# Optimization experiments

Measured on AMD Instinct MI355X. Metric: run time of the kernel, lower is better.

The kernel has to match this reference:

```python
import jax, jax.numpy as jnp
import numpy as np

P, B, N, M, D_LAT = 4, 32, 2048, 512, 128
BETA = 1e-3
BIG = 1e9  # sentinel for masked-out pairwise distances


def quat_to_rotmat(q):
    # q: (..., 4) quaternion (w, x, y, z), normalized then converted
    q = q / jnp.linalg.norm(q, axis=-1, keepdims=True)
    w, x, y, z = q[..., 0], q[..., 1], q[..., 2], q[..., 3]
    R = jnp.stack([
        1 - 2 * (y * y + z * z), 2 * (x * y - w * z), 2 * (x * z + w * y),
        2 * (x * y + w * z), 1 - 2 * (x * x + z * z), 2 * (y * z - w * x),
        2 * (x * z - w * y), 2 * (y * z + w * x), 1 - 2 * (x * x + y * y),
    ], axis=-1)
    return R.reshape(q.shape[:-1] + (3, 3))


def setup_inputs() -> dict:
    key = jax.random.key(0)
    ks = jax.random.split(key, 8)
    return {
        'ipt': jax.random.normal(ks[0], (B, N, 3), jnp.float32),
        'opt': jax.random.normal(ks[1], (P, B, M, 3), jnp.float32),
        'trans': jax.random.normal(ks[2], (P, B, 3), jnp.float32),
        'rots': jax.random.normal(ks[3], (P, B, 4), jnp.float32),
        'probs': jax.random.uniform(ks[4], (P, B, 1), jnp.float32),
        'idx': jax.random.randint(ks[5], (B, N), 0, P),
        'mu': jax.random.normal(ks[6], (B, D_LAT), jnp.float32),
        'logvar': jax.random.normal(ks[7], (B, D_LAT), jnp.float32),
    }


def _parts_distance(ipt, opt, trans, rots, probs, idx):
    # Masked, fully-batched equivalent of the original python double loop:
    # index_select by (idx==i) + _remove_zero_rows are expressed as boolean
    # masks; empty part/sample combinations are excluded via `valid`.
    chamfer_d = 0.0
    coverage = 0.0
    quality = 0.0
    num = 0.0
    nonzero_x = jnp.any(ipt != 0, axis=-1)  # (B, N)
    for i in range(P):  # fixed small part count, structurally distinct slices
        y = opt[i]                                   # (B, M, 3)
        mask_y = jnp.any(y != 0, axis=-1)            # (B, M) _remove_zero_rows
        mx = (idx == i) & nonzero_x                  # (B, N) part selection
        # transform_to_primitives_centric_system: x_local = R (x - t)
        R = quat_to_rotmat(rots[i])                  # (B, 3, 3)
        x = jnp.einsum('bij,bnj->bni', R, ipt - trans[i][:, None, :])
        # pairwise squared distances, (B, N, M)
        D = jnp.sum((x[:, :, None, :] - y[:, None, :, :]) ** 2, axis=-1)
        nx = jnp.sum(mx, axis=-1)                    # (B,)
        ny = jnp.sum(mask_y, axis=-1)                # (B,)
        # quality: mean over valid x of min distance to valid y
        qual = jnp.sum(jnp.where(mx, jnp.min(jnp.where(mask_y[:, None, :], D, BIG), axis=-1), 0.0), axis=-1) / jnp.maximum(nx, 1)
        # coverage: mean over valid y of min distance to valid x
        cov = jnp.sum(jnp.where(mask_y, jnp.min(jnp.where(mx[:, :, None], D, BIG), axis=-2), 0.0), axis=-1) / jnp.maximum(ny, 1)
        cd = qual + cov                              # symmetric chamfer
        valid = (nx > 0) & (ny > 0)                  # x.size(0)!=0 and y.size(0)!=0
        w = jnp.where(valid, probs[i][:, 0], 0.0)    # prob-weighted sum over batch
        n = jnp.sum(valid).astype(jnp.float32)
        has = (n > 0).astype(jnp.float32)
        inv_n = has / jnp.maximum(n, 1.0)
        chamfer_d = chamfer_d + jnp.sum(w * cd) * inv_n
        coverage = coverage + jnp.sum(w * cov) * inv_n
        quality = quality + jnp.sum(w * qual) * inv_n
        num = num + has
    inv_num = 1.0 / jnp.maximum(num, 1.0)
    return chamfer_d * inv_num, coverage * inv_num, quality * inv_num


def KL(mu, logvar):
    # standard VAE KL: sum over latent, mean over batch
    return -0.5 * jnp.sum(1.0 + logvar - mu ** 2 - jnp.exp(logvar)) / mu.shape[0]


def reference(ipt, opt, trans, rots, probs, idx, mu, logvar):
    cds, covs, quals = _parts_distance(ipt, opt, trans, rots, probs, idx)
    kld = KL(mu, logvar)
    return (cds + BETA * kld, cds, covs, quals, kld)
```

## Files before the change

kernel.cpp:

```cpp
#include <hip/hip_runtime.h>
#include <math.h>

#define PP 4
#define BB 32
#define PB (PP * BB)
#define NN 2048
#define MM 512
#define DLAT 128
#define BETA_C 1e-3f
#define BIGV 1e9f
#define SENT 1e8f
#define THREADS 512
#define NWAVE (THREADS / 64)
#define NCHUNK 2
#define QCH (NN / NCHUNK)
#define CCH (MM / NCHUNK)
#define XMAX (NN + 32)

__device__ float g_ws[8 * PB];

__device__ __forceinline__ int wave_compact_slot(bool sel, int* s_cnt, int tid) {
    unsigned long long bal = __ballot(sel);
    int lofs = __popcll(bal & ((1ull << (tid & 63)) - 1ull));
    int base = 0;
    if ((tid & 63) == 0 && bal) base = atomicAdd(s_cnt, __popcll(bal));
    base = __shfl(base, 0);
    return base + lofs;
}

__global__ __launch_bounds__(THREADS) void parts_kernel(
    const float* __restrict__ ipt,
    const float* __restrict__ opt,
    const float* __restrict__ trans,
    const float* __restrict__ rots,
    const int*   __restrict__ idx)
{
    const int b = blockIdx.x;
    const int i = blockIdx.y;
    const int z = blockIdx.z;
    const int tid = threadIdx.x;
    const int lane = tid & 63;
    const int w = tid >> 6;

    __shared__ float Rm[12];
    __shared__ int s_nx, s_ny;
    __shared__ __align__(16) float syx[MM], syy[MM], syz[MM];
    __shared__ __align__(16) float sxx[XMAX], sxy[XMAX], sxz[XMAX];
    __shared__ float pmin[NWAVE][256];
    __shared__ float red[NWAVE];

    if (tid == 0) {
        s_nx = 0;
        s_ny = 0;
        const float* q = rots + (i * BB + b) * 4;
        float qw = q[0], qx = q[1], qy = q[2], qz = q[3];
        float inv = 1.0f / sqrtf(qw * qw + qx * qx + qy * qy + qz * qz);
        qw *= inv; qx *= inv; qy *= inv; qz *= inv;
        Rm[0] = 1.0f - 2.0f * (qy * qy + qz * qz);
        Rm[1] = 2.0f * (qx * qy - qw * qz);
        Rm[2] = 2.0f * (qx * qz + qw * qy);
        Rm[3] = 2.0f * (qx * qy + qw * qz);
        Rm[4] = 1.0f - 2.0f * (qx * qx + qz * qz);
        Rm[5] = 2.0f * (qy * qz - qw * qx);
        Rm[6] = 2.0f * (qx * qz - qw * qy);
        Rm[7] = 2.0f * (qy * qz + qw * qx);
        Rm[8] = 1.0f - 2.0f * (qx * qx + qy * qy);
        const float* t = trans + (i * BB + b) * 3;
        Rm[9] = t[0]; Rm[10] = t[1]; Rm[11] = t[2];
    }
    __syncthreads();

    const float R0 = Rm[0], R1 = Rm[1], R2 = Rm[2];
    const float R3 = Rm[3], R4 = Rm[4], R5 = Rm[5];
    const float R6 = Rm[6], R7 = Rm[7], R8 = Rm[8];
    const float t0 = Rm[9], t1 = Rm[10], t2 = Rm[11];
    const size_t optbase = ((size_t)i * BB + b) * MM;
    const int pb = i * BB + b;

    float sum = 0.0f;

    if (z < NCHUNK) {
        for (int m = tid; m < MM; m += THREADS) {
            const float* y = opt + (optbase + m) * 3;
            float yx = y[0], yy = y[1], yz = y[2];
            bool v = (yx != 0.0f) | (yy != 0.0f) | (yz != 0.0f);
            if (!v) { yx = SENT; yy = SENT; yz = SENT; }
            syx[m] = yx; syy[m] = yy; syz[m] = yz;
        }
        const int n0 = z * QCH;
        for (int n = n0 + tid; n < n0 + QCH; n += THREADS) {
            const float* p = ipt + ((size_t)b * NN + n) * 3;
            float px = p[0], py = p[1], pz = p[2];
            bool nz = (px != 0.0f) | (py != 0.0f) | (pz != 0.0f);
            bool sel = nz && (idx[b * NN + n] == i);
            int pos = wave_compact_slot(sel, &s_nx, tid);
            if (sel) {
                px -= t0; py -= t1; pz -= t2;
                sxx[pos] = R0 * px + R1 * py + R2 * pz;
                sxy[pos] = R3 * px + R4 * py + R5 * pz;
                sxz[pos] = R6 * px + R7 * py + R8 * pz;
            }
        }
        __syncthreads();
        const int nxc = s_nx;
        const int y0 = w * (MM / NWAVE);

        for (int base = 0; base < nxc; base += 256) {
            float px[4], py[4], pz[4], mn[4];
#pragma unroll
            for (int s = 0; s < 4; ++s) {
                int k = base + s * 64 + lane;
                bool a = (k < nxc);
                px[s] = a ? sxx[k] : SENT;
                py[s] = a ? sxy[k] : SENT;
                pz[s] = a ? sxz[k] : SENT;
                mn[s] = BIGV;
            }
#pragma unroll 4
            for (int j = 0; j < MM / NWAVE; j += 4) {
                float4 yx = *reinterpret_cast<const float4*>(syx + y0 + j);
                float4 yy = *reinterpret_cast<const float4*>(syy + y0 + j);
                float4 yz = *reinterpret_cast<const float4*>(syz + y0 + j);
#pragma unroll
                for (int s = 0; s < 4; ++s) {
                    float dx0 = px[s] - yx.x, dy0 = py[s] - yy.x, dz0 = pz[s] - yz.x;
                    float dx1 = px[s] - yx.y, dy1 = py[s] - yy.y, dz1 = pz[s] - yz.y;
                    float dx2 = px[s] - yx.z, dy2 = py[s] - yy.z, dz2 = pz[s] - yz.z;
                    float dx3 = px[s] - yx.w, dy3 = py[s] - yy.w, dz3 = pz[s] - yz.w;
                    float d0 = dx0 * dx0 + dy0 * dy0 + dz0 * dz0;
                    float d1 = dx1 * dx1 + dy1 * dy1 + dz1 * dz1;
                    float d2 = dx2 * dx2 + dy2 * dy2 + dz2 * dz2;
                    float d3 = dx3 * dx3 + dy3 * dy3 + dz3 * dz3;
                    mn[s] = fminf(mn[s], fminf(fminf(d0, d1), fminf(d2, d3)));
                }
            }
#pragma unroll
            for (int s = 0; s < 4; ++s) pmin[w][s * 64 + lane] = mn[s];
            __syncthreads();
            if (tid < 256) {
                int j = tid;
                if (base + j < nxc) {
                    float m = pmin[0][j];
#pragma unroll
                    for (int ww = 1; ww < NWAVE; ++ww) m = fminf(m, pmin[ww][j]);
                    sum += m;
                }
            }
            __syncthreads();
        }

        for (int off = 32; off > 0; off >>= 1) sum += __shfl_down(sum, off);
        if (lane == 0) red[w] = sum;
        __syncthreads();
        if (tid == 0) {
            float tot = 0.0f;
            for (int ww = 0; ww < NWAVE; ++ww) tot += red[ww];
            g_ws[(0 + z) * PB + pb] = tot;
            g_ws[(4 + z) * PB + pb] = (float)s_nx;
        }
    } else {
        const int c = z - NCHUNK;
        if (tid < CCH) {
            const float* y = opt + (optbase + c * CCH + tid) * 3;
            float yx = y[0], yy = y[1], yz = y[2];
            bool v = (yx != 0.0f) | (yy != 0.0f) | (yz != 0.0f);
            if (!v) { yx = SENT; yy = SENT; yz = SENT; }
            syx[tid] = yx; syy[tid] = yy; syz[tid] = yz;
            unsigned long long bal = __ballot(v);
            if (lane == 0) atomicAdd(&s_ny, __popcll(bal));
        }
        for (int n = tid; n < NN; n += THREADS) {
            const float* p = ipt + ((size_t)b * NN + n) * 3;
            float px = p[0], py = p[1], pz = p[2];
            bool nz = (px != 0.0f) | (py != 0.0f) | (pz != 0.0f);
            bool sel = nz && (idx[b * NN + n] == i);
            int pos = wave_compact_slot(sel, &s_nx, tid);
            if (sel) {
                px -= t0; py -= t1; pz -= t2;
                sxx[pos] = R0 * px + R1 * py + R2 * pz;
                sxy[pos] = R3 * px + R4 * py + R5 * pz;
                sxz[pos] = R6 * px + R7 * py + R8 * pz;
            }
        }
        __syncthreads();
        const int nx = s_nx;
        const int ny = s_ny;
        const int nx32 = (nx + 31) & ~31;
        if (tid < nx32 - nx) {
            sxx[nx + tid] = SENT; sxy[nx + tid] = SENT; sxz[nx + tid] = SENT;
        }
        __syncthreads();

        float qx[4], qy[4], qz[4], mn[4];
#pragma unroll
        for (int s = 0; s < 4; ++s) {
            int j = s * 64 + lane;
            qx[s] = syx[j]; qy[s] = syy[j]; qz[s] = syz[j];
            mn[s] = BIGV;
        }
        const int q = nx32 / NWAVE;
        const int x0 = w * q;
#pragma unroll 4
        for (int k = 0; k < q; k += 4) {
            float4 xx = *reinterpret_cast<const float4*>(sxx + x0 + k);
            float4 xy = *reinterpret_cast<const float4*>(sxy + x0 + k);
            float4 xz = *reinterpret_cast<const float4*>(sxz + x0 + k);
#pragma unroll
            for (int s = 0; s < 4; ++s) {
                float dx0 = qx[s] - xx.x, dy0 = qy[s] - xy.x, dz0 = qz[s] - xz.x;
                float dx1 = qx[s] - xx.y, dy1 = qy[s] - xy.y, dz1 = qz[s] - xz.y;
                float dx2 = qx[s] - xx.z, dy2 = qy[s] - xy.z, dz2 = qz[s] - xz.z;
                float dx3 = qx[s] - xx.w, dy3 = qy[s] - xy.w, dz3 = qz[s] - xz.w;
                float d0 = dx0 * dx0 + dy0 * dy0 + dz0 * dz0;
                float d1 = dx1 * dx1 + dy1 * dy1 + dz1 * dz1;
                float d2 = dx2 * dx2 + dy2 * dy2 + dz2 * dz2;
                float d3 = dx3 * dx3 + dy3 * dy3 + dz3 * dz3;
                mn[s] = fminf(mn[s], fminf(fminf(d0, d1), fminf(d2, d3)));
            }
        }
#pragma unroll
        for (int s = 0; s < 4; ++s) pmin[w][s * 64 + lane] = mn[s];
        __syncthreads();
        if (tid < CCH) {
            int j = tid;
            if (syx[j] != SENT) {
                float m = pmin[0][j];
#pragma unroll
                for (int ww = 1; ww < NWAVE; ++ww) m = fminf(m, pmin[ww][j]);
                sum += m;
            }
        }
        __syncthreads();

        for (int off = 32; off > 0; off >>= 1) sum += __shfl_down(sum, off);
        if (lane == 0) red[w] = sum;
        __syncthreads();
        if (tid == 0) {
            float tot = 0.0f;
            for (int ww = 0; ww < NWAVE; ++ww) tot += red[ww];
            g_ws[(2 + c) * PB + pb] = tot;
            g_ws[(6 + c) * PB + pb] = (float)ny;
        }
    }
}

__global__ __launch_bounds__(256) void finalize_kernel(
    const float* __restrict__ probs,
    const float* __restrict__ mu,
    const float* __restrict__ logvar,
    float* __restrict__ out)
{
    const int tid = threadIdx.x;
    __shared__ float red[4];
    __shared__ float s_wq[PB], s_wc[PB], s_val[PB];

    const float4* mu4 = reinterpret_cast<const float4*>(mu);
    const float4* lv4 = reinterpret_cast<const float4*>(logvar);
    float kls = 0.0f;
    for (int t = tid; t < BB * DLAT / 4; t += 256) {
        float4 m4 = mu4[t], l4 = lv4[t];
        kls += (1.0f + l4.x - m4.x * m4.x - expf(l4.x))
             + (1.0f + l4.y - m4.y * m4.y - expf(l4.y))
             + (1.0f + l4.z - m4.z * m4.z - expf(l4.z))
             + (1.0f + l4.w - m4.w * m4.w - expf(l4.w));
    }
    for (int off = 32; off > 0; off >>= 1) kls += __shfl_down(kls, off);
    if ((tid & 63) == 0) red[tid >> 6] = kls;

    if (tid < PB) {
        float qs  = g_ws[0 * PB + tid] + g_ws[1 * PB + tid];
        float cs  = g_ws[2 * PB + tid] + g_ws[3 * PB + tid];
        float nxf = g_ws[4 * PB + tid] + g_ws[5 * PB + tid];
        float nyf = g_ws[6 * PB + tid] + g_ws[7 * PB + tid];
        bool valid = (nxf > 0.0f) && (nyf > 0.0f);
        float w = valid ? probs[tid] : 0.0f;
        s_wq[tid] = w * (qs / fmaxf(nxf, 1.0f));
        s_wc[tid] = w * (cs / fmaxf(nyf, 1.0f));
        s_val[tid] = valid ? 1.0f : 0.0f;
    }
    __syncthreads();

    if (tid == 0) {
        float kld = -0.5f * (red[0] + red[1] + red[2] + red[3]) / (float)BB;
        float ch = 0.0f, cov = 0.0f, qu = 0.0f, num = 0.0f;
        for (int i = 0; i < PP; ++i) {
            float sq = 0.0f, sc = 0.0f, n = 0.0f;
            for (int bb = 0; bb < BB; ++bb) {
                sq += s_wq[i * BB + bb];
                sc += s_wc[i * BB + bb];
                n += s_val[i * BB + bb];
            }
            float has = (n > 0.0f) ? 1.0f : 0.0f;
            float invn = has / fmaxf(n, 1.0f);
            qu += sq * invn;
            cov += sc * invn;
            ch += (sq + sc) * invn;
            num += has;
        }
        float invnum = 1.0f / fmaxf(num, 1.0f);
        float cds = ch * invnum;
        out[0] = cds + BETA_C * kld;
        out[1] = cds;
        out[2] = cov * invnum;
        out[3] = qu * invnum;
        out[4] = kld;
    }
}

extern "C" void kernel_launch(void* const* d_in, const int* in_sizes, int n_in,
                              void* d_out, int out_size, void* d_ws, size_t ws_size,
                              hipStream_t stream) {
    const float* ipt    = (const float*)d_in[0];
    const float* opt    = (const float*)d_in[1];
    const float* trans  = (const float*)d_in[2];
    const float* rots   = (const float*)d_in[3];
    const float* probs  = (const float*)d_in[4];
    const int*   idx    = (const int*)d_in[5];
    const float* mu     = (const float*)d_in[6];
    const float* logvar = (const float*)d_in[7];
    float* out = (float*)d_out;
    (void)d_ws; (void)ws_size; (void)in_sizes; (void)n_in; (void)out_size;

    dim3 grid(BB, PP, 2 * NCHUNK);
    parts_kernel<<<grid, THREADS, 0, stream>>>(ipt, opt, trans, rots, idx);
    finalize_kernel<<<1, 256, 0, stream>>>(probs, mu, logvar, out);
}
```

Baseline: 95.23 us.

## Fuse finalize into parts kernel via last-block atomic and split work finer

Merges the finalize kernel into the main kernel: each block bumps a global counter after a threadfence, and the last block to finish does the KL and weighted reduction. This removes a second launch and its gap. The grid also goes from 4 to 8 chunks per (part, batch), with 256-thread blocks and 2 points per lane instead of 4, to raise block count and occupancy. The cost is more redundant per-block loading and compaction of the input points, plus the atomic-counter handshake.

```diff
diff --git a/kernel.cpp b/kernel.cpp
--- a/kernel.cpp
+++ b/kernel.cpp
@@ -10,30 +10,37 @@
 #define BETA_C 1e-3f
 #define BIGV 1e9f
 #define SENT 1e8f
-#define THREADS 512
-#define NWAVE (THREADS / 64)
-#define NCHUNK 2
-#define QCH (NN / NCHUNK)
-#define CCH (MM / NCHUNK)
-#define XMAX (NN + 32)
-
-__device__ float g_ws[8 * PB];
-
-__device__ __forceinline__ int wave_compact_slot(bool sel, int* s_cnt, int tid) {
+#define THREADS 256
+#define NWAVE 4
+#define QCHUNKS 4
+#define CCHUNKS 4
+#define QCH (NN / QCHUNKS)
+#define CCH (MM / CCHUNKS)
+#define TOTALBLK (BB * PP * (QCHUNKS + CCHUNKS))
+#define XMAX (NN + 16)
+
+__device__ float g_ws[16 * PB];
+__device__ int g_done;
+
+__device__ __forceinline__ int wave_compact_slot(bool sel, int* s_cnt, int lane) {
     unsigned long long bal = __ballot(sel);
-    int lofs = __popcll(bal & ((1ull << (tid & 63)) - 1ull));
+    int lofs = __popcll(bal & ((1ull << lane) - 1ull));
     int base = 0;
-    if ((tid & 63) == 0 && bal) base = atomicAdd(s_cnt, __popcll(bal));
+    if (lane == 0 && bal) base = atomicAdd(s_cnt, __popcll(bal));
     base = __shfl(base, 0);
     return base + lofs;
 }
 
-__global__ __launch_bounds__(THREADS) void parts_kernel(
+__global__ __launch_bounds__(THREADS) void fused_kernel(
     const float* __restrict__ ipt,
     const float* __restrict__ opt,
     const float* __restrict__ trans,
     const float* __restrict__ rots,
-    const int*   __restrict__ idx)
+    const int*   __restrict__ idx,
+    const float* __restrict__ probs,
+    const float* __restrict__ mu,
+    const float* __restrict__ logvar,
+    float* __restrict__ out)
 {
     const int b = blockIdx.x;
     const int i = blockIdx.y;
@@ -43,10 +50,10 @@
     const int w = tid >> 6;
 
     __shared__ float Rm[12];
-    __shared__ int s_nx, s_ny;
+    __shared__ int s_nx, s_ny, s_last;
     __shared__ __align__(16) float syx[MM], syy[MM], syz[MM];
     __shared__ __align__(16) float sxx[XMAX], sxy[XMAX], sxz[XMAX];
-    __shared__ float pmin[NWAVE][256];
+    __shared__ float pmin[NWAVE][128];
     __shared__ float red[NWAVE];
 
     if (tid == 0) {
@@ -79,7 +86,7 @@
 
     float sum = 0.0f;
 
-    if (z < NCHUNK) {
+    if (z < QCHUNKS) {
         for (int m = tid; m < MM; m += THREADS) {
             const float* y = opt + (optbase + m) * 3;
             float yx = y[0], yy = y[1], yz = y[2];
@@ -93,7 +100,7 @@
             float px = p[0], py = p[1], pz = p[2];
             bool nz = (px != 0.0f) | (py != 0.0f) | (pz != 0.0f);
             bool sel = nz && (idx[b * NN + n] == i);
-            int pos = wave_compact_slot(sel, &s_nx, tid);
+            int pos = wave_compact_slot(sel, &s_nx, lane);
             if (sel) {
                 px -= t0; py -= t1; pz -= t2;
                 sxx[pos] = R0 * px + R1 * py + R2 * pz;
@@ -105,24 +112,24 @@
         const int nxc = s_nx;
         const int y0 = w * (MM / NWAVE);
 
-        for (int base = 0; base < nxc; base += 256) {
-            float px[4], py[4], pz[4], mn[4];
-#pragma unroll
-            for (int s = 0; s < 4; ++s) {
+        for (int base = 0; base < nxc; base += 128) {
+            float px[2], py[2], pz[2], mn[2];
+            bool act[2];
+#pragma unroll
+            for (int s = 0; s < 2; ++s) {
                 int k = base + s * 64 + lane;
-                bool a = (k < nxc);
-                px[s] = a ? sxx[k] : SENT;
-                py[s] = a ? sxy[k] : SENT;
-                pz[s] = a ? sxz[k] : SENT;
+                act[s] = (k < nxc);
+                px[s] = act[s] ? sxx[k] : SENT;
+                py[s] = act[s] ? sxy[k] : SENT;
+                pz[s] = act[s] ? sxz[k] : SENT;
                 mn[s] = BIGV;
             }
-#pragma unroll 4
             for (int j = 0; j < MM / NWAVE; j += 4) {
                 float4 yx = *reinterpret_cast<const float4*>(syx + y0 + j);
                 float4 yy = *reinterpret_cast<const float4*>(syy + y0 + j);
                 float4 yz = *reinterpret_cast<const float4*>(syz + y0 + j);
 #pragma unroll
-                for (int s = 0; s < 4; ++s) {
+                for (int s = 0; s < 2; ++s) {
                     float dx0 = px[s] - yx.x, dy0 = py[s] - yy.x, dz0 = pz[s] - yz.x;
                     float dx1 = px[s] - yx.y, dy1 = py[s] - yy.y, dz1 = pz[s] - yz.y;
                     float dx2 = px[s] - yx.z, dy2 = py[s] - yy.z, dz2 = pz[s] - yz.z;
@@ -135,16 +142,13 @@
                 }
             }
 #pragma unroll
-            for (int s = 0; s < 4; ++s) pmin[w][s * 64 + lane] = mn[s];
+            for (int s = 0; s < 2; ++s) pmin[w][s * 64 + lane] = mn[s];
             __syncthreads();
-            if (tid < 256) {
-                int j = tid;
-                if (base + j < nxc) {
-                    float m = pmin[0][j];
-#pragma unroll
-                    for (int ww = 1; ww < NWAVE; ++ww) m = fminf(m, pmin[ww][j]);
-                    sum += m;
-                }
+            if (tid < 128 && base + tid < nxc) {
+                float m = pmin[0][tid];
+#pragma unroll
+                for (int ww = 1; ww < NWAVE; ++ww) m = fminf(m, pmin[ww][tid]);
+                sum += m;
             }
             __syncthreads();
         }
@@ -153,13 +157,12 @@
         if (lane == 0) red[w] = sum;
         __syncthreads();
         if (tid == 0) {
-            float tot = 0.0f;
-            for (int ww = 0; ww < NWAVE; ++ww) tot += red[ww];
+            float tot = red[0] + red[1] + red[2] + red[3];
             g_ws[(0 + z) * PB + pb] = tot;
-            g_ws[(4 + z) * PB + pb] = (float)s_nx;
+            g_ws[(8 + z) * PB + pb] = (float)s_nx;
         }
     } else {
-        const int c = z - NCHUNK;
+        const int c = z - QCHUNKS;
         if (tid < CCH) {
             const float* y = opt + (optbase + c * CCH + tid) * 3;
             float yx = y[0], yy = y[1], yz = y[2];
@@ -174,7 +177,7 @@
             float px = p[0], py = p[1], pz = p[2];
             bool nz = (px != 0.0f) | (py != 0.0f) | (pz != 0.0f);
             bool sel = nz && (idx[b * NN + n] == i);
-            int pos = wave_compact_slot(sel, &s_nx, tid);
+            int pos = wave_compact_slot(sel, &s_nx, lane);
             if (sel) {
                 px -= t0; py -= t1; pz -= t2;
                 sxx[pos] = R0 * px + R1 * py + R2 * pz;
@@ -185,28 +188,27 @@
         __syncthreads();
         const int nx = s_nx;
         const int ny = s_ny;
-        const int nx32 = (nx + 31) & ~31;
-        if (tid < nx32 - nx) {
+        const int nx16 = (nx + 15) & ~15;
+        if (tid < nx16 - nx) {
             sxx[nx + tid] = SENT; sxy[nx + tid] = SENT; sxz[nx + tid] = SENT;
         }
         __syncthreads();
 
-        float qx[4], qy[4], qz[4], mn[4];
-#pragma unroll
-        for (int s = 0; s < 4; ++s) {
+        float qx[2], qy[2], qz[2], mn[2];
+#pragma unroll
+        for (int s = 0; s < 2; ++s) {
             int j = s * 64 + lane;
             qx[s] = syx[j]; qy[s] = syy[j]; qz[s] = syz[j];
             mn[s] = BIGV;
         }
-        const int q = nx32 / NWAVE;
+        const int q = nx16 / NWAVE;
         const int x0 = w * q;
-#pragma unroll 4
         for (int k = 0; k < q; k += 4) {
             float4 xx = *reinterpret_cast<const float4*>(sxx + x0 + k);
             float4 xy = *reinterpret_cast<const float4*>(sxy + x0 + k);
             float4 xz = *reinterpret_cast<const float4*>(sxz + x0 + k);
 #pragma unroll
-            for (int s = 0; s < 4; ++s) {
+            for (int s = 0; s < 2; ++s) {
                 float dx0 = qx[s] - xx.x, dy0 = qy[s] - xy.x, dz0 = qz[s] - xz.x;
                 float dx1 = qx[s] - xx.y, dy1 = qy[s] - xy.y, dz1 = qz[s] - xz.y;
                 float dx2 = qx[s] - xx.z, dy2 = qy[s] - xy.z, dz2 = qz[s] - xz.z;
@@ -219,16 +221,13 @@
             }
         }
 #pragma unroll
-        for (int s = 0; s < 4; ++s) pmin[w][s * 64 + lane] = mn[s];
-        __syncthreads();
-        if (tid < CCH) {
-            int j = tid;
-            if (syx[j] != SENT) {
-                float m = pmin[0][j];
-#pragma unroll
-                for (int ww = 1; ww < NWAVE; ++ww) m = fminf(m, pmin[ww][j]);
-                sum += m;
-            }
+        for (int s = 0; s < 2; ++s) pmin[w][s * 64 + lane] = mn[s];
+        __syncthreads();
+        if (tid < CCH && syx[tid] != SENT) {
+            float m = pmin[0][tid];
+#pragma unroll
+            for (int ww = 1; ww < NWAVE; ++ww) m = fminf(m, pmin[ww][tid]);
+            sum += m;
         }
         __syncthreads();
 
@@ -236,28 +235,26 @@
         if (lane == 0) red[w] = sum;
         __syncthreads();
         if (tid == 0) {
-            float tot = 0.0f;
-            for (int ww = 0; ww < NWAVE; ++ww) tot += red[ww];
-            g_ws[(2 + c) * PB + pb] = tot;
-            g_ws[(6 + c) * PB + pb] = (float)ny;
-        }
-    }
-}
-
-__global__ __launch_bounds__(256) void finalize_kernel(
-    const float* __restrict__ probs,
-    const float* __restrict__ mu,
-    const float* __restrict__ logvar,
-    float* __restrict__ out)
-{
-    const int tid = threadIdx.x;
-    __shared__ float red[4];
-    __shared__ float s_wq[PB], s_wc[PB], s_val[PB];
+            float tot = red[0] + red[1] + red[2] + red[3];
+            g_ws[(4 + c) * PB + pb] = tot;
+            g_ws[(12 + c) * PB + pb] = (float)ny;
+        }
+    }
+
+    __threadfence();
+    if (tid == 0) {
+        int prev = atomicAdd(&g_done, 1);
+        s_last = (prev == TOTALBLK - 1) ? 1 : 0;
+        if (s_last) atomicExch(&g_done, 0);
+    }
+    __syncthreads();
+    if (!s_last) return;
+    __threadfence();
 
     const float4* mu4 = reinterpret_cast<const float4*>(mu);
     const float4* lv4 = reinterpret_cast<const float4*>(logvar);
     float kls = 0.0f;
-    for (int t = tid; t < BB * DLAT / 4; t += 256) {
+    for (int t = tid; t < BB * DLAT / 4; t += THREADS) {
         float4 m4 = mu4[t], l4 = lv4[t];
         kls += (1.0f + l4.x - m4.x * m4.x - expf(l4.x))
              + (1.0f + l4.y - m4.y * m4.y - expf(l4.y))
@@ -265,17 +262,20 @@
              + (1.0f + l4.w - m4.w * m4.w - expf(l4.w));
     }
     for (int off = 32; off > 0; off >>= 1) kls += __shfl_down(kls, off);
-    if ((tid & 63) == 0) red[tid >> 6] = kls;
-
+    if (lane == 0) red[w] = kls;
+
+    float* s_wq = syx;
+    float* s_wc = syy;
+    float* s_val = syz;
     if (tid < PB) {
-        float qs  = g_ws[0 * PB + tid] + g_ws[1 * PB + tid];
-        float cs  = g_ws[2 * PB + tid] + g_ws[3 * PB + tid];
-        float nxf = g_ws[4 * PB + tid] + g_ws[5 * PB + tid];
-        float nyf = g_ws[6 * PB + tid] + g_ws[7 * PB + tid];
+        float qs  = g_ws[0 * PB + tid] + g_ws[1 * PB + tid] + g_ws[2 * PB + tid] + g_ws[3 * PB + tid];
+        float cs  = g_ws[4 * PB + tid] + g_ws[5 * PB + tid] + g_ws[6 * PB + tid] + g_ws[7 * PB + tid];
+        float nxf = g_ws[8 * PB + tid] + g_ws[9 * PB + tid] + g_ws[10 * PB + tid] + g_ws[11 * PB + tid];
+        float nyf = g_ws[12 * PB + tid] + g_ws[13 * PB + tid] + g_ws[14 * PB + tid] + g_ws[15 * PB + tid];
         bool valid = (nxf > 0.0f) && (nyf > 0.0f);
-        float w = valid ? probs[tid] : 0.0f;
-        s_wq[tid] = w * (qs / fmaxf(nxf, 1.0f));
-        s_wc[tid] = w * (cs / fmaxf(nyf, 1.0f));
+        float wgt = valid ? probs[tid] : 0.0f;
+        s_wq[tid] = wgt * (qs / fmaxf(nxf, 1.0f));
+        s_wc[tid] = wgt * (cs / fmaxf(nyf, 1.0f));
         s_val[tid] = valid ? 1.0f : 0.0f;
     }
     __syncthreads();
@@ -283,12 +283,12 @@
     if (tid == 0) {
         float kld = -0.5f * (red[0] + red[1] + red[2] + red[3]) / (float)BB;
         float ch = 0.0f, cov = 0.0f, qu = 0.0f, num = 0.0f;
-        for (int i = 0; i < PP; ++i) {
+        for (int ii = 0; ii < PP; ++ii) {
             float sq = 0.0f, sc = 0.0f, n = 0.0f;
             for (int bb = 0; bb < BB; ++bb) {
-                sq += s_wq[i * BB + bb];
-                sc += s_wc[i * BB + bb];
-                n += s_val[i * BB + bb];
+                sq += s_wq[ii * BB + bb];
+                sc += s_wc[ii * BB + bb];
+                n += s_val[ii * BB + bb];
             }
             float has = (n > 0.0f) ? 1.0f : 0.0f;
             float invn = has / fmaxf(n, 1.0f);
@@ -321,7 +321,7 @@
     float* out = (float*)d_out;
     (void)d_ws; (void)ws_size; (void)in_sizes; (void)n_in; (void)out_size;
 
-    dim3 grid(BB, PP, 2 * NCHUNK);
-    parts_kernel<<<grid, THREADS, 0, stream>>>(ipt, opt, trans, rots, idx);
-    finalize_kernel<<<1, 256, 0, stream>>>(probs, mu, logvar, out);
+    dim3 grid(BB, PP, QCHUNKS + CCHUNKS);
+    fused_kernel<<<grid, THREADS, 0, stream>>>(ipt, opt, trans, rots, idx,
+                                               probs, mu, logvar, out);
 }
```

After: 158.0 us. 1.66x slower.
